# Kernel optimization log

Hardware: AMD Instinct MI355X
Metric: run time of the kernel (lower is better)

The kernel has to match this reference:

```python
import jax, jax.numpy as jnp
import numpy as np

N, NFEAT, NHID, NCLASS, NHEADS = 4096, 512, 64, 40, 8
ALPHA = 0.2
NEG = -9e15


def setup_inputs() -> dict:
    key = jax.random.key(0)
    ks = jax.random.split(key, 6)
    x = jax.random.normal(ks[0], (N, NFEAT), dtype=jnp.float32)
    adj = jax.random.randint(ks[1], (2, N, N), 0, 2, dtype=jnp.int32)
    # Xavier-ish scaled params
    W1 = jax.random.normal(ks[2], (NHEADS, NFEAT, NHID), dtype=jnp.float32) * (1.0 / np.sqrt(NFEAT))
    a1 = jax.random.normal(ks[3], (NHEADS, 2, NHID), dtype=jnp.float32) * (1.0 / np.sqrt(2 * NHID))
    Wo = jax.random.normal(ks[4], (NHEADS * NHID, NCLASS), dtype=jnp.float32) * (1.0 / np.sqrt(NHEADS * NHID))
    ao = jax.random.normal(ks[5], (2, NCLASS), dtype=jnp.float32) * (1.0 / np.sqrt(2 * NCLASS))
    return {"x": x, "adj": adj, "W1": W1, "a1": a1, "Wo": Wo, "ao": ao}


def _gat_layer(h, adj_mask, W, a_src, a_dst, concat):
    # h: [N,F]; W: [...,F,F']; a_src/a_dst: [...,F']
    if W.ndim == 3:  # multi-head: [H,F,F']
        Wh = jnp.einsum('nf,hfd->hnd', h, W)              # [H,N,F']
        f1 = jnp.einsum('hnd,hd->hn', Wh, a_src)           # [H,N]
        f2 = jnp.einsum('hnd,hd->hn', Wh, a_dst)
        e = jax.nn.leaky_relu(f1[:, :, None] + f2[:, None, :], ALPHA)  # [H,N,N]
        e = jnp.where(adj_mask[None], e, NEG)
        att = jax.nn.softmax(e, axis=-1)
        out = jnp.einsum('hnm,hmd->hnd', att, Wh)          # [H,N,F']
    else:
        Wh = h @ W                                         # [N,F']
        f1 = Wh @ a_src
        f2 = Wh @ a_dst
        e = jax.nn.leaky_relu(f1[:, None] + f2[None, :], ALPHA)
        e = jnp.where(adj_mask, e, NEG)
        att = jax.nn.softmax(e, axis=-1)
        out = att @ Wh
    return jax.nn.elu(out) if concat else out


def reference(x, adj, W1, a1, Wo, ao):
    adj1 = adj[1] > 0
    adj0 = adj[0] > 0
    # layer 1: NHEADS heads, concat=True
    h = _gat_layer(x, adj1, W1, a1[:, 0], a1[:, 1], concat=True)   # [H,N,NHID]
    h = jnp.transpose(h, (1, 0, 2)).reshape(x.shape[0], -1)        # [N, H*NHID]
    # output layer: concat=False, then outer ELU + log_softmax
    out = _gat_layer(h, adj0, Wo, ao[0], ao[1], concat=False)      # [N, NCLASS]
    out = jax.nn.elu(out)
    return jax.nn.log_softmax(out, axis=1)
```

## Files before the change

kernel.cpp:

```cpp
#include <hip/hip_runtime.h>
#include <hip/hip_bf16.h>

#define N      4096
#define NFEAT  512
#define NHID   64
#define NHEADS 8
#define NCLASS 40
#define ALPHA  0.2f
#define LOG2E  1.44269504f

typedef unsigned short u16;
typedef unsigned int   u32;
typedef __attribute__((ext_vector_type(8))) short bf16x8;
typedef __attribute__((ext_vector_type(4))) float f32x4;

__device__ __forceinline__ float b2f(u16 u) {
    return __uint_as_float(((u32)u) << 16);
}
__device__ __forceinline__ u32 rnd_hi(float f) {
    u32 u = __float_as_uint(f);
    return u + 0x7FFFu + ((u >> 16) & 1u);
}
__device__ __forceinline__ u32 pk2(float lo, float hi) {
    __hip_bfloat162 h = __float22bfloat162_rn(make_float2(lo, hi));
    return *(u32*)&h;
}
__device__ __forceinline__ u16 f2b(float f) {
    return (u16)(rnd_hi(f) >> 16);
}
__device__ __forceinline__ float mexp(int m, float t) {
    return m ? __builtin_amdgcn_exp2f(fmaxf(t, ALPHA * t)) : 0.f;
}
__device__ __forceinline__ bf16x8 ones_frag() {
    union { u16 u[8]; bf16x8 v; } o;
    #pragma unroll
    for (int j = 0; j < 8; ++j) o.u[j] = 0x3F80;
    return o.v;
}

__global__ __launch_bounds__(256) void kcx(const float* __restrict__ x,
                                           u16* __restrict__ xb) {
    const int g = blockIdx.x * 256 + threadIdx.x;
    const size_t base = (size_t)g * 8;
    float4 v0 = *(const float4*)&x[base];
    float4 v1 = *(const float4*)&x[base + 4];
    uint4 o;
    o.x = pk2(v0.x, v0.y); o.y = pk2(v0.z, v0.w);
    o.z = pk2(v1.x, v1.y); o.w = pk2(v1.z, v1.w);
    *(uint4*)&xb[base] = o;
}

__global__ __launch_bounds__(256) void kcw(const float* __restrict__ W1,
                                           u16* __restrict__ W1b) {
    __shared__ float ts[64 * 68];
    const int t  = threadIdx.x;
    const int f0 = blockIdx.x * 64;
    const int h  = blockIdx.y;
    #pragma unroll
    for (int i = 0; i < 4; ++i) {
        int flat = t + 256 * i;
        int row = flat >> 4;
        int c4  = (flat & 15) * 4;
        *(float4*)&ts[row * 68 + c4] =
            *(const float4*)&W1[((size_t)h * 512 + f0 + row) * 64 + c4];
    }
    __syncthreads();
    const int d  = t >> 2;
    const int fs = (t & 3) * 16;
    u32 p[8];
    #pragma unroll
    for (int j = 0; j < 8; ++j)
        p[j] = pk2(ts[(fs + 2 * j) * 68 + d], ts[(fs + 2 * j + 1) * 68 + d]);
    u32* dst = (u32*)&W1b[((size_t)(h * 64 + d)) * 512 + f0 + fs];
    *(uint4*)dst       = make_uint4(p[0], p[1], p[2], p[3]);
    *(uint4*)(dst + 4) = make_uint4(p[4], p[5], p[6], p[7]);
}

__global__ __launch_bounds__(256, 4) void k1m_gemm1(const u16* __restrict__ xb,
                                                    const u16* __restrict__ W1b,
                                                    const float* __restrict__ a1,
                                                    u16* __restrict__ Wh1T,
                                                    float* __restrict__ F1,
                                                    float* __restrict__ F2) {
    __shared__ u16 xs[64 * 72];
    __shared__ u16 wvs[64 * 72];
    const int t    = threadIdx.x;
    const int n0   = blockIdx.x * 64;
    const int h    = blockIdx.y;
    const int lane = t & 63;
    const int l15  = lane & 15;
    const int q    = lane >> 4;
    const int wrow = (t >> 6) * 16;
    f32x4 acc[4];
    #pragma unroll
    for (int df = 0; df < 4; ++df)
        #pragma unroll
        for (int r = 0; r < 4; ++r) acc[df][r] = 0.f;
    for (int f0 = 0; f0 < 512; f0 += 64) {
        uint4 sx[2], sw[2];
        #pragma unroll
        for (int i = 0; i < 2; ++i) {
            int flat = t + 256 * i;
            int row = flat >> 3;
            int c8  = (flat & 7) * 8;
            sx[i] = *(const uint4*)&xb[(size_t)(n0 + row) * 512 + f0 + c8];
            sw[i] = *(const uint4*)&W1b[((size_t)(h * 64 + row)) * 512 + f0 + c8];
        }
        __syncthreads();
        #pragma unroll
        for (int i = 0; i < 2; ++i) {
            int flat = t + 256 * i;
            int row = flat >> 3;
            int c8  = (flat & 7) * 8;
            *(uint4*)&xs[row * 72 + c8]  = sx[i];
            *(uint4*)&wvs[row * 72 + c8] = sw[i];
        }
        __syncthreads();
        #pragma unroll
        for (int ks = 0; ks < 2; ++ks) {
            int k0 = ks * 32 + q * 8;
            bf16x8 a = *(const bf16x8*)&xs[(wrow + l15) * 72 + k0];
            #pragma unroll
            for (int df = 0; df < 4; ++df) {
                bf16x8 b = *(const bf16x8*)&wvs[(df * 16 + l15) * 72 + k0];
                acc[df] = __builtin_amdgcn_mfma_f32_16x16x32_bf16(a, b, acc[df], 0, 0, 0);
            }
        }
    }
    #pragma unroll
    for (int df = 0; df < 4; ++df) {
        uint2 o;
        o.x = pk2(acc[df][0], acc[df][1]);
        o.y = pk2(acc[df][2], acc[df][3]);
        *(uint2*)&Wh1T[((size_t)(h * 64 + df * 16 + l15)) * 4096 + n0 + wrow + q * 4] = o;
    }
    float a1v[4], a2v[4];
    #pragma unroll
    for (int df = 0; df < 4; ++df) {
        a1v[df] = a1[h * 128 + df * 16 + l15];
        a2v[df] = a1[h * 128 + 64 + df * 16 + l15];
    }
    #pragma unroll
    for (int r = 0; r < 4; ++r) {
        float s1 = 0.f, s2 = 0.f;
        #pragma unroll
        for (int df = 0; df < 4; ++df) {
            s1 += acc[df][r] * a1v[df];
            s2 += acc[df][r] * a2v[df];
        }
        #pragma unroll
        for (int off = 8; off >= 1; off >>= 1) {
            s1 += __shfl_xor(s1, off);
            s2 += __shfl_xor(s2, off);
        }
        if (l15 == 0) {
            int n = n0 + wrow + q * 4 + r;
            F1[h * 4096 + n] = s1 * LOG2E;
            F2[h * 4096 + n] = s2 * LOG2E;
        }
    }
}

__global__ __launch_bounds__(256, 4) void k3_attn1(const int* __restrict__ adj1,
                                                   const u16* __restrict__ Wh1T,
                                                   const float* __restrict__ F1,
                                                   const float* __restrict__ F2,
                                                   float* __restrict__ pacc1,
                                                   float* __restrict__ pz1) {
    __shared__ u16  wbf[64 * 136];
    __shared__ u16  whT[64 * 136];
    __shared__ float f1s[64];
    const int t     = threadIdx.x;
    const int n0    = blockIdx.x * 64;
    const int h     = blockIdx.y;
    const int chunk = blockIdx.z;
    const int lane  = t & 63;
    const int l15   = lane & 15;
    const int q     = lane >> 4;
    const int wrow  = (t >> 6) * 16;
    const int c4    = (t & 31) * 4;
    const int rg    = t >> 5;
    const bf16x8 bones = ones_frag();
    if (t < 64) f1s[t] = F1[h * N + n0 + t];
    f32x4 acc[5];
    #pragma unroll
    for (int df = 0; df < 5; ++df)
        #pragma unroll
        for (int r = 0; r < 4; ++r) acc[df][r] = 0.f;

    const int mbeg = chunk * 2048;
    int4 aprev[8];
    #pragma unroll
    for (int i = 0; i < 8; ++i)
        aprev[i] = *(const int4*)&adj1[(size_t)(n0 + rg + 8 * i) * N + mbeg + c4];
    __syncthreads();

    for (int m0 = mbeg; m0 < mbeg + 2048; m0 += 128) {
        float4 F2v = *(const float4*)&F2[h * N + m0 + c4];
        #pragma unroll
        for (int i = 0; i < 8; ++i) {
            int rr = rg + 8 * i;
            int4 a4 = aprev[i];
            float f1v = f1s[rr];
            float w0 = mexp(a4.x, f1v + F2v.x);
            float w1 = mexp(a4.y, f1v + F2v.y);
            float w2 = mexp(a4.z, f1v + F2v.z);
            float w3 = mexp(a4.w, f1v + F2v.w);
            uint2 pk;
            pk.x = pk2(w0, w1);
            pk.y = pk2(w2, w3);
            *(uint2*)&wbf[rr * 136 + c4] = pk;
        }
        int mn = (m0 + 128 < mbeg + 2048) ? m0 + 128 : mbeg;
        #pragma unroll
        for (int i = 0; i < 8; ++i)
            aprev[i] = *(const int4*)&adj1[(size_t)(n0 + rg + 8 * i) * N + mn + c4];
        #pragma unroll
        for (int i = 0; i < 4; ++i) {
            int flat = t + 256 * i;
            int row = flat >> 4;
            int c8  = (flat & 15) * 8;
            *(uint4*)&whT[row * 136 + c8] =
                *(const uint4*)&Wh1T[((size_t)(h * 64 + row)) * 4096 + m0 + c8];
        }
        __syncthreads();
        #pragma unroll
        for (int ks = 0; ks < 4; ++ks) {
            int k0 = ks * 32 + q * 8;
            bf16x8 a = *(const bf16x8*)&wbf[(wrow + l15) * 136 + k0];
            #pragma unroll
            for (int df = 0; df < 4; ++df) {
                bf16x8 b = *(const bf16x8*)&whT[(df * 16 + l15) * 136 + k0];
                acc[df] = __builtin_amdgcn_mfma_f32_16x16x32_bf16(a, b, acc[df], 0, 0, 0);
            }
            acc[4] = __builtin_amdgcn_mfma_f32_16x16x32_bf16(a, bones, acc[4], 0, 0, 0);
        }
        __syncthreads();
    }
    const size_t rowbase = (size_t)(chunk * 8 + h) * 4096 + n0;
    #pragma unroll
    for (int r = 0; r < 4; ++r) {
        int nl = wrow + q * 4 + r;
        if (l15 == 0) pz1[rowbase + nl] = acc[4][r];
        #pragma unroll
        for (int df = 0; df < 4; ++df)
            pacc1[(rowbase + nl) * 64 + df * 16 + l15] = acc[df][r];
    }
}

__global__ __launch_bounds__(256) void k3b_norm(const float* __restrict__ pacc1,
                                                const float* __restrict__ pz1,
                                                float* __restrict__ h1) {
    const int g = blockIdx.x * 256 + threadIdx.x;
    const int d = g & 63;
    const int h = (g >> 6) & 7;
    const int n = g >> 9;
    const size_t i0 = (size_t)h * 4096 + n;
    float s = pacc1[i0 * 64 + d] + pacc1[(i0 + 8 * 4096) * 64 + d];
    float z = pz1[i0] + pz1[i0 + 8 * 4096];
    float v = s / fmaxf(z, 1e-30f);
    h1[(size_t)n * 512 + h * 64 + d] = v > 0.f ? v : __expf(v) - 1.f;
}

__global__ __launch_bounds__(256) void k4_gemm2(const float* __restrict__ h1,
                                                const float* __restrict__ Wo,
                                                const float* __restrict__ ao,
                                                float* __restrict__ F1o,
                                                float* __restrict__ F2o,
                                                u16* __restrict__ Wh2T) {
    const int t = threadIdx.x;
    const int c = t & 63;
    const int n = blockIdx.x * 4 + (t >> 6);
    float acc = 0.f;
    if (c < NCLASS) {
        const float* hrow = &h1[(size_t)n * 512];
        #pragma unroll 8
        for (int f = 0; f < 512; ++f)
            acc += hrow[f] * Wo[f * NCLASS + c];
        Wh2T[(size_t)c * 4096 + n] = f2b(acc);
    }
    float s1 = (c < NCLASS) ? acc * ao[c] : 0.f;
    float s2 = (c < NCLASS) ? acc * ao[NCLASS + c] : 0.f;
    #pragma unroll
    for (int off = 32; off >= 1; off >>= 1) {
        s1 += __shfl_xor(s1, off);
        s2 += __shfl_xor(s2, off);
    }
    if (c == 0) {
        F1o[n] = s1 * LOG2E;
        F2o[n] = s2 * LOG2E;
    }
}

__global__ __launch_bounds__(256, 5) void k5a_attn2(const int* __restrict__ adj0,
                                                    const u16* __restrict__ Wh2T,
                                                    const float* __restrict__ F1o,
                                                    const float* __restrict__ F2o,
                                                    float* __restrict__ pacc,
                                                    float* __restrict__ pz) {
    __shared__ u16  wbf[64 * 136];
    __shared__ u16  whT[48 * 136];
    __shared__ float f1s[64];
    const int t     = threadIdx.x;
    const int n0    = blockIdx.x * 64;
    const int chunk = blockIdx.y;
    const int mbase = chunk * 256;
    const int lane  = t & 63;
    const int l15   = lane & 15;
    const int q     = lane >> 4;
    const int wrow  = (t >> 6) * 16;
    const int c4    = (t & 31) * 4;
    const int rg    = t >> 5;
    const bf16x8 bones = ones_frag();
    if (t < 64) f1s[t] = F1o[n0 + t];
    #pragma unroll
    for (int i = 0; i < 5; ++i) {
        int idx = t + 256 * i;
        if (idx < 1088) whT[40 * 136 + idx] = 0;
    }
    f32x4 acc[4];
    #pragma unroll
    for (int df = 0; df < 4; ++df)
        #pragma unroll
        for (int r = 0; r < 4; ++r) acc[df][r] = 0.f;
    int4 aprev[8];
    #pragma unroll
    for (int i = 0; i < 8; ++i)
        aprev[i] = *(const int4*)&adj0[(size_t)(n0 + rg + 8 * i) * N + mbase + c4];
    __syncthreads();

    for (int mt = 0; mt < 2; ++mt) {
        int m0 = mbase + mt * 128;
        float4 F2v = *(const float4*)&F2o[m0 + c4];
        #pragma unroll
        for (int i = 0; i < 8; ++i) {
            int rr = rg + 8 * i;
            int4 a4 = aprev[i];
            float f1v = f1s[rr];
            float w0 = mexp(a4.x, f1v + F2v.x);
            float w1 = mexp(a4.y, f1v + F2v.y);
            float w2 = mexp(a4.z, f1v + F2v.z);
            float w3 = mexp(a4.w, f1v + F2v.w);
            uint2 pk;
            pk.x = pk2(w0, w1);
            pk.y = pk2(w2, w3);
            *(uint2*)&wbf[rr * 136 + c4] = pk;
        }
        int mn = mbase + ((mt + 1) & 1) * 128;
        #pragma unroll
        for (int i = 0; i < 8; ++i)
            aprev[i] = *(const int4*)&adj0[(size_t)(n0 + rg + 8 * i) * N + mn + c4];
        #pragma unroll
        for (int i = 0; i < 3; ++i) {
            int flat = t + 256 * i;
            if (flat < 640) {
                int row = flat >> 4;
                int c8  = (flat & 15) * 8;
                *(uint4*)&whT[row * 136 + c8] =
                    *(const uint4*)&Wh2T[(size_t)row * 4096 + m0 + c8];
            }
        }
        __syncthreads();
        #pragma unroll
        for (int ks = 0; ks < 4; ++ks) {
            int k0 = ks * 32 + q * 8;
            bf16x8 a = *(const bf16x8*)&wbf[(wrow + l15) * 136 + k0];
            #pragma unroll
            for (int df = 0; df < 3; ++df) {
                bf16x8 b = *(const bf16x8*)&whT[(df * 16 + l15) * 136 + k0];
                acc[df] = __builtin_amdgcn_mfma_f32_16x16x32_bf16(a, b, acc[df], 0, 0, 0);
            }
            acc[3] = __builtin_amdgcn_mfma_f32_16x16x32_bf16(a, bones, acc[3], 0, 0, 0);
        }
        __syncthreads();
    }
    #pragma unroll
    for (int r = 0; r < 4; ++r) {
        int n = n0 + wrow + q * 4 + r;
        if (l15 == 0) pz[(size_t)chunk * N + n] = acc[3][r];
        #pragma unroll
        for (int df = 0; df < 3; ++df) {
            int c = df * 16 + l15;
            if (c < NCLASS)
                pacc[((size_t)chunk * N + n) * NCLASS + c] = acc[df][r];
        }
    }
}

__global__ __launch_bounds__(256) void k5b_final(const float* __restrict__ pacc,
                                                 const float* __restrict__ pz,
                                                 float* __restrict__ out) {
    const int t = threadIdx.x;
    const int lane = t & 63;
    const int n = blockIdx.x * 4 + (t >> 6);
    float s = 0.f, Z = 0.f;
    #pragma unroll
    for (int ch = 0; ch < 16; ++ch) {
        Z += pz[(size_t)ch * N + n];
        if (lane < NCLASS) s += pacc[(size_t)(ch * N + n) * NCLASS + lane];
    }
    float v;
    if (lane < NCLASS) {
        v = s / fmaxf(Z, 1e-30f);
        v = v > 0.f ? v : __expf(v) - 1.f;
    } else {
        v = -INFINITY;
    }
    float mx = v;
    #pragma unroll
    for (int off = 32; off >= 1; off >>= 1) mx = fmaxf(mx, __shfl_xor(mx, off));
    float ex = (lane < NCLASS) ? __expf(v - mx) : 0.f;
    #pragma unroll
    for (int off = 32; off >= 1; off >>= 1) ex += __shfl_xor(ex, off);
    float lse = mx + __logf(ex);
    if (lane < NCLASS) out[(size_t)n * NCLASS + lane] = v - lse;
}

extern "C" void kernel_launch(void* const* d_in, const int* in_sizes, int n_in,
                              void* d_out, int out_size, void* d_ws, size_t ws_size,
                              hipStream_t stream) {
    const float* x   = (const float*)d_in[0];
    const int*   adj = (const int*)d_in[1];
    const float* W1  = (const float*)d_in[2];
    const float* a1  = (const float*)d_in[3];
    const float* Wo  = (const float*)d_in[4];
    const float* ao  = (const float*)d_in[5];

    float* ws    = (float*)d_ws;
    float* h1    = ws;
    float* F1    = h1 + 2097152;
    float* F2    = F1 + 32768;
    float* F1o   = F2 + 32768;
    float* F2o   = F1o + 4096;
    float* pz    = F2o + 4096;
    float* pz1   = pz + 65536;
    u16*   Wh1T  = (u16*)(pz1 + 65536);
    u16*   Wh2T  = Wh1T + 2097152;
    float* R     = (float*)(Wh2T + 163840);
    u16*   xb    = (u16*)R;
    u16*   W1b   = xb + 2097152;
    float* pacc1 = R;
    float* pacc  = R;

    const int* adj0 = adj;
    const int* adj1 = adj + (size_t)N * N;

    hipLaunchKernelGGL(kcx,       dim3(1024),     dim3(256), 0, stream, x, xb);
    hipLaunchKernelGGL(kcw,       dim3(8, 8),     dim3(256), 0, stream, W1, W1b);
    hipLaunchKernelGGL(k1m_gemm1, dim3(64, 8),    dim3(256), 0, stream, xb, W1b, a1, Wh1T, F1, F2);
    hipLaunchKernelGGL(k3_attn1,  dim3(64, 8, 2), dim3(256), 0, stream, adj1, Wh1T, F1, F2, pacc1, pz1);
    hipLaunchKernelGGL(k3b_norm,  dim3(8192),     dim3(256), 0, stream, pacc1, pz1, h1);
    hipLaunchKernelGGL(k4_gemm2,  dim3(1024),     dim3(256), 0, stream, h1, Wo, ao, F1o, F2o, Wh2T);
    hipLaunchKernelGGL(k5a_attn2, dim3(64, 16),   dim3(256), 0, stream, adj0, Wh2T, F1o, F2o, pacc, pz);
    hipLaunchKernelGGL(k5b_final, dim3(1024),     dim3(256), 0, stream, pacc, pz, (float*)d_out);
}
```

Baseline: 333.5 us.

## Compute attention weights directly in MFMA A-fragment registers, skipping LDS staging

In both attention kernels each lane now loads the adjacency entries matching its own MFMA A-operand slot, computes the exponentiated weights in registers and packs them straight into bf16x8 fragments. This removes the shared-memory round trip for the weight tile. The Wh tile is prefetched into registers one step ahead, and F2 is cached in LDS for the whole chunk. Adjacency reads per lane become 32-byte row segments rather than coalesced 128-column strips, which may cost memory efficiency. The attn2 launch bound drops to 4 blocks per SM.

```diff
diff --git a/kernel.cpp b/kernel.cpp
--- a/kernel.cpp
+++ b/kernel.cpp
@@ -167,9 +167,8 @@
                                                    const float* __restrict__ F2,
                                                    float* __restrict__ pacc1,
                                                    float* __restrict__ pz1) {
-    __shared__ u16  wbf[64 * 136];
-    __shared__ u16  whT[64 * 136];
-    __shared__ float f1s[64];
+    __shared__ u16   whT[64 * 136];
+    __shared__ float f2s[2048];
     const int t     = threadIdx.x;
     const int n0    = blockIdx.x * 64;
     const int h     = blockIdx.y;
@@ -178,62 +177,78 @@
     const int l15   = lane & 15;
     const int q     = lane >> 4;
     const int wrow  = (t >> 6) * 16;
-    const int c4    = (t & 31) * 4;
-    const int rg    = t >> 5;
+    const int row   = wrow + l15;
     const bf16x8 bones = ones_frag();
-    if (t < 64) f1s[t] = F1[h * N + n0 + t];
+    const int mbeg  = chunk * 2048;
+    const float f1v = F1[h * N + n0 + row];
+
+    {
+        float4 fa = *(const float4*)&F2[h * N + mbeg + t * 8];
+        float4 fb = *(const float4*)&F2[h * N + mbeg + t * 8 + 4];
+        *(float4*)&f2s[t * 8]     = fa;
+        *(float4*)&f2s[t * 8 + 4] = fb;
+    }
+
+    const int srow = t >> 4;
+    const int sc8  = (t & 15) * 8;
+    const u16* wbase = Wh1T + ((size_t)(h * 64 + srow)) * 4096 + sc8;
+    const int* adjq  = adj1 + (size_t)(n0 + row) * N + q * 8;
+
+    uint4 bw[4];
+    int4  aj[4][2];
+    auto pref_bw = [&](int m0) {
+        #pragma unroll
+        for (int i = 0; i < 4; ++i)
+            bw[i] = *(const uint4*)(wbase + (size_t)(16 * i) * 4096 + m0);
+    };
+    auto pref_adj = [&](int m0) {
+        #pragma unroll
+        for (int ks = 0; ks < 4; ++ks) {
+            aj[ks][0] = *(const int4*)(adjq + m0 + ks * 32);
+            aj[ks][1] = *(const int4*)(adjq + m0 + ks * 32 + 4);
+        }
+    };
+
     f32x4 acc[5];
     #pragma unroll
     for (int df = 0; df < 5; ++df)
         #pragma unroll
         for (int r = 0; r < 4; ++r) acc[df][r] = 0.f;
 
-    const int mbeg = chunk * 2048;
-    int4 aprev[8];
-    #pragma unroll
-    for (int i = 0; i < 8; ++i)
-        aprev[i] = *(const int4*)&adj1[(size_t)(n0 + rg + 8 * i) * N + mbeg + c4];
-    __syncthreads();
-
-    for (int m0 = mbeg; m0 < mbeg + 2048; m0 += 128) {
-        float4 F2v = *(const float4*)&F2[h * N + m0 + c4];
-        #pragma unroll
-        for (int i = 0; i < 8; ++i) {
-            int rr = rg + 8 * i;
-            int4 a4 = aprev[i];
-            float f1v = f1s[rr];
-            float w0 = mexp(a4.x, f1v + F2v.x);
-            float w1 = mexp(a4.y, f1v + F2v.y);
-            float w2 = mexp(a4.z, f1v + F2v.z);
-            float w3 = mexp(a4.w, f1v + F2v.w);
-            uint2 pk;
-            pk.x = pk2(w0, w1);
-            pk.y = pk2(w2, w3);
-            *(uint2*)&wbf[rr * 136 + c4] = pk;
-        }
-        int mn = (m0 + 128 < mbeg + 2048) ? m0 + 128 : mbeg;
-        #pragma unroll
-        for (int i = 0; i < 8; ++i)
-            aprev[i] = *(const int4*)&adj1[(size_t)(n0 + rg + 8 * i) * N + mn + c4];
-        #pragma unroll
-        for (int i = 0; i < 4; ++i) {
-            int flat = t + 256 * i;
-            int row = flat >> 4;
-            int c8  = (flat & 15) * 8;
-            *(uint4*)&whT[row * 136 + c8] =
-                *(const uint4*)&Wh1T[((size_t)(h * 64 + row)) * 4096 + m0 + c8];
-        }
-        __syncthreads();
-        #pragma unroll
-        for (int ks = 0; ks < 4; ++ks) {
-            int k0 = ks * 32 + q * 8;
-            bf16x8 a = *(const bf16x8*)&wbf[(wrow + l15) * 136 + k0];
+    pref_bw(mbeg);
+    pref_adj(mbeg);
+
+    for (int it = 0; it < 16; ++it) {
+        const int mrel  = it * 128;
+        const int mnext = mbeg + ((it < 15) ? mrel + 128 : 0);
+        #pragma unroll
+        for (int i = 0; i < 4; ++i)
+            *(uint4*)&whT[(srow + 16 * i) * 136 + sc8] = bw[i];
+        __syncthreads();
+        pref_bw(mnext);
+        bf16x8 af[4];
+        #pragma unroll
+        for (int ks = 0; ks < 4; ++ks) {
+            const float* f2p = &f2s[mrel + ks * 32 + q * 8];
+            float4 fa = *(const float4*)f2p;
+            float4 fb = *(const float4*)(f2p + 4);
+            int4 a0 = aj[ks][0], a1 = aj[ks][1];
+            union { u32 u[4]; bf16x8 v; } fr;
+            fr.u[0] = pk2(mexp(a0.x, f1v + fa.x), mexp(a0.y, f1v + fa.y));
+            fr.u[1] = pk2(mexp(a0.z, f1v + fa.z), mexp(a0.w, f1v + fa.w));
+            fr.u[2] = pk2(mexp(a1.x, f1v + fb.x), mexp(a1.y, f1v + fb.y));
+            fr.u[3] = pk2(mexp(a1.z, f1v + fb.z), mexp(a1.w, f1v + fb.w));
+            af[ks] = fr.v;
+        }
+        pref_adj(mnext);
+        #pragma unroll
+        for (int ks = 0; ks < 4; ++ks) {
             #pragma unroll
             for (int df = 0; df < 4; ++df) {
-                bf16x8 b = *(const bf16x8*)&whT[(df * 16 + l15) * 136 + k0];
-                acc[df] = __builtin_amdgcn_mfma_f32_16x16x32_bf16(a, b, acc[df], 0, 0, 0);
+                bf16x8 b = *(const bf16x8*)&whT[(df * 16 + l15) * 136 + ks * 32 + q * 8];
+                acc[df] = __builtin_amdgcn_mfma_f32_16x16x32_bf16(af[ks], b, acc[df], 0, 0, 0);
             }
-            acc[4] = __builtin_amdgcn_mfma_f32_16x16x32_bf16(a, bones, acc[4], 0, 0, 0);
+            acc[4] = __builtin_amdgcn_mfma_f32_16x16x32_bf16(af[ks], bones, acc[4], 0, 0, 0);
         }
         __syncthreads();
     }
@@ -292,15 +307,14 @@
     }
 }
 
-__global__ __launch_bounds__(256, 5) void k5a_attn2(const int* __restrict__ adj0,
+__global__ __launch_bounds__(256, 4) void k5a_attn2(const int* __restrict__ adj0,
                                                     const u16* __restrict__ Wh2T,
                                                     const float* __restrict__ F1o,
                                                     const float* __restrict__ F2o,
                                                     float* __restrict__ pacc,
                                                     float* __restrict__ pz) {
-    __shared__ u16  wbf[64 * 136];
-    __shared__ u16  whT[48 * 136];
-    __shared__ float f1s[64];
+    __shared__ u16   whT[48 * 136];
+    __shared__ float f2s[256];
     const int t     = threadIdx.x;
     const int n0    = blockIdx.x * 64;
     const int chunk = blockIdx.y;
@@ -309,68 +323,80 @@
     const int l15   = lane & 15;
     const int q     = lane >> 4;
     const int wrow  = (t >> 6) * 16;
-    const int c4    = (t & 31) * 4;
-    const int rg    = t >> 5;
+    const int row   = wrow + l15;
     const bf16x8 bones = ones_frag();
-    if (t < 64) f1s[t] = F1o[n0 + t];
+    const float f1v = F1o[n0 + row];
+
+    if (t < 64) *(float4*)&f2s[t * 4] = *(const float4*)&F2o[mbase + t * 4];
     #pragma unroll
     for (int i = 0; i < 5; ++i) {
         int idx = t + 256 * i;
         if (idx < 1088) whT[40 * 136 + idx] = 0;
     }
+
+    const int srow = t >> 4;
+    const int sc8  = (t & 15) * 8;
+    const u16* wbase = Wh2T + (size_t)srow * 4096 + sc8;
+    const int* adjq  = adj0 + (size_t)(n0 + row) * N + q * 8;
+
+    uint4 bw[3];
+    int4  aj[4][2];
+    auto pref_bw = [&](int m0) {
+        #pragma unroll
+        for (int i = 0; i < 3; ++i)
+            if (srow + 16 * i < 40)
+                bw[i] = *(const uint4*)(wbase + (size_t)(16 * i) * 4096 + m0);
+    };
+    auto pref_adj = [&](int m0) {
+        #pragma unroll
+        for (int ks = 0; ks < 4; ++ks) {
+            aj[ks][0] = *(const int4*)(adjq + m0 + ks * 32);
+            aj[ks][1] = *(const int4*)(adjq + m0 + ks * 32 + 4);
+        }
+    };
+
     f32x4 acc[4];
     #pragma unroll
     for (int df = 0; df < 4; ++df)
         #pragma unroll
         for (int r = 0; r < 4; ++r) acc[df][r] = 0.f;
-    int4 aprev[8];
-    #pragma unroll
-    for (int i = 0; i < 8; ++i)
-        aprev[i] = *(const int4*)&adj0[(size_t)(n0 + rg + 8 * i) * N + mbase + c4];
-    __syncthreads();
-
+
+    pref_bw(mbase);
+    pref_adj(mbase);
+
+    #pragma unroll
     for (int mt = 0; mt < 2; ++mt) {
-        int m0 = mbase + mt * 128;
-        float4 F2v = *(const float4*)&F2o[m0 + c4];
-        #pragma unroll
-        for (int i = 0; i < 8; ++i) {
-            int rr = rg + 8 * i;
-            int4 a4 = aprev[i];
-            float f1v = f1s[rr];
-            float w0 = mexp(a4.x, f1v + F2v.x);
-            float w1 = mexp(a4.y, f1v + F2v.y);
-            float w2 = mexp(a4.z, f1v + F2v.z);
-            float w3 = mexp(a4.w, f1v + F2v.w);
-            uint2 pk;
-            pk.x = pk2(w0, w1);
-            pk.y = pk2(w2, w3);
-            *(uint2*)&wbf[rr * 136 + c4] = pk;
-        }
-        int mn = mbase + ((mt + 1) & 1) * 128;
-        #pragma unroll
-        for (int i = 0; i < 8; ++i)
-            aprev[i] = *(const int4*)&adj0[(size_t)(n0 + rg + 8 * i) * N + mn + c4];
-        #pragma unroll
-        for (int i = 0; i < 3; ++i) {
-            int flat = t + 256 * i;
-            if (flat < 640) {
-                int row = flat >> 4;
-                int c8  = (flat & 15) * 8;
-                *(uint4*)&whT[row * 136 + c8] =
-                    *(const uint4*)&Wh2T[(size_t)row * 4096 + m0 + c8];
-            }
-        }
-        __syncthreads();
-        #pragma unroll
-        for (int ks = 0; ks < 4; ++ks) {
-            int k0 = ks * 32 + q * 8;
-            bf16x8 a = *(const bf16x8*)&wbf[(wrow + l15) * 136 + k0];
+        const int mrel  = mt * 128;
+        const int mnext = mbase + ((mt + 1) & 1) * 128;
+        #pragma unroll
+        for (int i = 0; i < 3; ++i)
+            if (srow + 16 * i < 40)
+                *(uint4*)&whT[(srow + 16 * i) * 136 + sc8] = bw[i];
+        __syncthreads();
+        pref_bw(mnext);
+        bf16x8 af[4];
+        #pragma unroll
+        for (int ks = 0; ks < 4; ++ks) {
+            const float* f2p = &f2s[mrel + ks * 32 + q * 8];
+            float4 fa = *(const float4*)f2p;
+            float4 fb = *(const float4*)(f2p + 4);
+            int4 a0 = aj[ks][0], a1 = aj[ks][1];
+            union { u32 u[4]; bf16x8 v; } fr;
+            fr.u[0] = pk2(mexp(a0.x, f1v + fa.x), mexp(a0.y, f1v + fa.y));
+            fr.u[1] = pk2(mexp(a0.z, f1v + fa.z), mexp(a0.w, f1v + fa.w));
+            fr.u[2] = pk2(mexp(a1.x, f1v + fb.x), mexp(a1.y, f1v + fb.y));
+            fr.u[3] = pk2(mexp(a1.z, f1v + fb.z), mexp(a1.w, f1v + fb.w));
+            af[ks] = fr.v;
+        }
+        pref_adj(mnext);
+        #pragma unroll
+        for (int ks = 0; ks < 4; ++ks) {
             #pragma unroll
             for (int df = 0; df < 3; ++df) {
-                bf16x8 b = *(const bf16x8*)&whT[(df * 16 + l15) * 136 + k0];
-                acc[df] = __builtin_amdgcn_mfma_f32_16x16x32_bf16(a, b, acc[df], 0, 0, 0);
+                bf16x8 b = *(const bf16x8*)&whT[(df * 16 + l15) * 136 + ks * 32 + q * 8];
+                acc[df] = __builtin_amdgcn_mfma_f32_16x16x32_bf16(af[ks], b, acc[df], 0, 0, 0);
             }
-            acc[3] = __builtin_amdgcn_mfma_f32_16x16x32_bf16(a, bones, acc[3], 0, 0, 0);
+            acc[3] = __builtin_amdgcn_mfma_f32_16x16x32_bf16(af[ks], bones, acc[3], 0, 0, 0);
         }
         __syncthreads();
     }
```

After: 402.8 us. +20.8%, slower.

## Register-prefetch next tile and use raw barriers without vmcnt drain

Applied to the files above, without the earlier changes.

In the projection kernel and both attention kernels, the next iteration's global loads (x/W tiles, Wh tiles, adjacency, F2) are now issued into registers before the current tile's MFMA work. __syncthreads is replaced by an lgkmcnt wait plus s_barrier fenced with sched_barrier, so the barrier no longer waits for outstanding global loads and those loads can overlap compute. This adds register pressure, and k5a_attn2's launch bounds occupancy hint drops from 5 to 4 to make room.

```diff
diff --git a/kernel.cpp b/kernel.cpp
--- a/kernel.cpp
+++ b/kernel.cpp
@@ -96,26 +96,33 @@
     for (int df = 0; df < 4; ++df)
         #pragma unroll
         for (int r = 0; r < 4; ++r) acc[df][r] = 0.f;
+
+    uint4 sx[2], sw[2];
+    const int srow = t >> 3;
+    const int sc8  = (t & 7) * 8;
+    const u16* xb0 = xb + (size_t)(n0 + srow) * 512 + sc8;
+    const u16* wb0 = W1b + ((size_t)(h * 64 + srow)) * 512 + sc8;
+    #pragma unroll
+    for (int i = 0; i < 2; ++i) {
+        sx[i] = *(const uint4*)(xb0 + (size_t)(32 * i) * 512);
+        sw[i] = *(const uint4*)(wb0 + (size_t)(32 * i) * 512);
+    }
     for (int f0 = 0; f0 < 512; f0 += 64) {
-        uint4 sx[2], sw[2];
         #pragma unroll
         for (int i = 0; i < 2; ++i) {
-            int flat = t + 256 * i;
-            int row = flat >> 3;
-            int c8  = (flat & 7) * 8;
-            sx[i] = *(const uint4*)&xb[(size_t)(n0 + row) * 512 + f0 + c8];
-            sw[i] = *(const uint4*)&W1b[((size_t)(h * 64 + row)) * 512 + f0 + c8];
-        }
-        __syncthreads();
+            *(uint4*)&xs[(srow + 32 * i) * 72 + sc8]  = sx[i];
+            *(uint4*)&wvs[(srow + 32 * i) * 72 + sc8] = sw[i];
+        }
+        const int fn = (f0 + 64 < 512) ? f0 + 64 : 0;
         #pragma unroll
         for (int i = 0; i < 2; ++i) {
-            int flat = t + 256 * i;
-            int row = flat >> 3;
-            int c8  = (flat & 7) * 8;
-            *(uint4*)&xs[row * 72 + c8]  = sx[i];
-            *(uint4*)&wvs[row * 72 + c8] = sw[i];
-        }
-        __syncthreads();
+            sx[i] = *(const uint4*)(xb0 + (size_t)(32 * i) * 512 + fn);
+            sw[i] = *(const uint4*)(wb0 + (size_t)(32 * i) * 512 + fn);
+        }
+        asm volatile("s_waitcnt lgkmcnt(0)" ::: "memory");
+        __builtin_amdgcn_sched_barrier(0);
+        __builtin_amdgcn_s_barrier();
+        __builtin_amdgcn_sched_barrier(0);
         #pragma unroll
         for (int ks = 0; ks < 2; ++ks) {
             int k0 = ks * 32 + q * 8;
@@ -126,6 +133,9 @@
                 acc[df] = __builtin_amdgcn_mfma_f32_16x16x32_bf16(a, b, acc[df], 0, 0, 0);
             }
         }
+        __builtin_amdgcn_sched_barrier(0);
+        __builtin_amdgcn_s_barrier();
+        __builtin_amdgcn_sched_barrier(0);
     }
     #pragma unroll
     for (int df = 0; df < 4; ++df) {
@@ -180,27 +190,41 @@
     const int wrow  = (t >> 6) * 16;
     const int c4    = (t & 31) * 4;
     const int rg    = t >> 5;
+    const int srow  = t >> 4;
+    const int sc8   = (t & 15) * 8;
     const bf16x8 bones = ones_frag();
+    const int mbeg  = chunk * 2048;
     if (t < 64) f1s[t] = F1[h * N + n0 + t];
-    f32x4 acc[5];
+
+    const u16*   wb0  = Wh1T + ((size_t)(h * 64 + srow)) * 4096 + sc8;
+    const int*   adjp = adj1 + (size_t)(n0 + rg) * N + c4;
+    const float* f2p  = F2 + (size_t)h * N + c4;
+
+    uint4  bw[4];
+    int4   aj[8];
+    float4 f2n;
+    f32x4  acc[5];
     #pragma unroll
     for (int df = 0; df < 5; ++df)
         #pragma unroll
         for (int r = 0; r < 4; ++r) acc[df][r] = 0.f;
 
-    const int mbeg = chunk * 2048;
-    int4 aprev[8];
+    #pragma unroll
+    for (int i = 0; i < 4; ++i)
+        bw[i] = *(const uint4*)(wb0 + (size_t)(16 * i) * 4096 + mbeg);
     #pragma unroll
     for (int i = 0; i < 8; ++i)
-        aprev[i] = *(const int4*)&adj1[(size_t)(n0 + rg + 8 * i) * N + mbeg + c4];
+        aj[i] = *(const int4*)(adjp + (size_t)(8 * i) * N + mbeg);
+    f2n = *(const float4*)(f2p + mbeg);
     __syncthreads();
 
-    for (int m0 = mbeg; m0 < mbeg + 2048; m0 += 128) {
-        float4 F2v = *(const float4*)&F2[h * N + m0 + c4];
+    for (int it = 0; it < 16; ++it) {
+        const int m0 = mbeg + it * 128;
+        const float4 F2v = f2n;
         #pragma unroll
         for (int i = 0; i < 8; ++i) {
             int rr = rg + 8 * i;
-            int4 a4 = aprev[i];
+            int4 a4 = aj[i];
             float f1v = f1s[rr];
             float w0 = mexp(a4.x, f1v + F2v.x);
             float w1 = mexp(a4.y, f1v + F2v.y);
@@ -211,19 +235,21 @@
             pk.y = pk2(w2, w3);
             *(uint2*)&wbf[rr * 136 + c4] = pk;
         }
-        int mn = (m0 + 128 < mbeg + 2048) ? m0 + 128 : mbeg;
+        #pragma unroll
+        for (int i = 0; i < 4; ++i)
+            *(uint4*)&whT[(srow + 16 * i) * 136 + sc8] = bw[i];
+        const int mn = (it < 15) ? m0 + 128 : mbeg;
+        #pragma unroll
+        for (int i = 0; i < 4; ++i)
+            bw[i] = *(const uint4*)(wb0 + (size_t)(16 * i) * 4096 + mn);
         #pragma unroll
         for (int i = 0; i < 8; ++i)
-            aprev[i] = *(const int4*)&adj1[(size_t)(n0 + rg + 8 * i) * N + mn + c4];
-        #pragma unroll
-        for (int i = 0; i < 4; ++i) {
-            int flat = t + 256 * i;
-            int row = flat >> 4;
-            int c8  = (flat & 15) * 8;
-            *(uint4*)&whT[row * 136 + c8] =
-                *(const uint4*)&Wh1T[((size_t)(h * 64 + row)) * 4096 + m0 + c8];
-        }
-        __syncthreads();
+            aj[i] = *(const int4*)(adjp + (size_t)(8 * i) * N + mn);
+        f2n = *(const float4*)(f2p + mn);
+        asm volatile("s_waitcnt lgkmcnt(0)" ::: "memory");
+        __builtin_amdgcn_sched_barrier(0);
+        __builtin_amdgcn_s_barrier();
+        __builtin_amdgcn_sched_barrier(0);
         #pragma unroll
         for (int ks = 0; ks < 4; ++ks) {
             int k0 = ks * 32 + q * 8;
@@ -235,7 +261,9 @@
             }
             acc[4] = __builtin_amdgcn_mfma_f32_16x16x32_bf16(a, bones, acc[4], 0, 0, 0);
         }
-        __syncthreads();
+        __builtin_amdgcn_sched_barrier(0);
+        __builtin_amdgcn_s_barrier();
+        __builtin_amdgcn_sched_barrier(0);
     }
     const size_t rowbase = (size_t)(chunk * 8 + h) * 4096 + n0;
     #pragma unroll
@@ -292,7 +320,7 @@
     }
 }
 
-__global__ __launch_bounds__(256, 5) void k5a_attn2(const int* __restrict__ adj0,
+__global__ __launch_bounds__(256, 4) void k5a_attn2(const int* __restrict__ adj0,
                                                     const u16* __restrict__ Wh2T,
                                                     const float* __restrict__ F1o,
                                                     const float* __restrict__ F2o,
@@ -311,6 +339,8 @@
     const int wrow  = (t >> 6) * 16;
     const int c4    = (t & 31) * 4;
     const int rg    = t >> 5;
+    const int srow  = t >> 4;
+    const int sc8   = (t & 15) * 8;
     const bf16x8 bones = ones_frag();
     if (t < 64) f1s[t] = F1o[n0 + t];
     #pragma unroll
@@ -318,24 +348,37 @@
         int idx = t + 256 * i;
         if (idx < 1088) whT[40 * 136 + idx] = 0;
     }
-    f32x4 acc[4];
+
+    const u16*   wb0  = Wh2T + (size_t)srow * 4096 + sc8;
+    const int*   adjp = adj0 + (size_t)(n0 + rg) * N + c4;
+    const float* f2p  = F2o + c4;
+
+    uint4  bw[3];
+    int4   aj[8];
+    float4 f2n;
+    f32x4  acc[4];
     #pragma unroll
     for (int df = 0; df < 4; ++df)
         #pragma unroll
         for (int r = 0; r < 4; ++r) acc[df][r] = 0.f;
-    int4 aprev[8];
+
+    #pragma unroll
+    for (int i = 0; i < 3; ++i)
+        if (srow + 16 * i < 40)
+            bw[i] = *(const uint4*)(wb0 + (size_t)(16 * i) * 4096 + mbase);
     #pragma unroll
     for (int i = 0; i < 8; ++i)
-        aprev[i] = *(const int4*)&adj0[(size_t)(n0 + rg + 8 * i) * N + mbase + c4];
+        aj[i] = *(const int4*)(adjp + (size_t)(8 * i) * N + mbase);
+    f2n = *(const float4*)(f2p + mbase);
     __syncthreads();
 
+    #pragma unroll
     for (int mt = 0; mt < 2; ++mt) {
-        int m0 = mbase + mt * 128;
-        float4 F2v = *(const float4*)&F2o[m0 + c4];
+        const float4 F2v = f2n;
         #pragma unroll
         for (int i = 0; i < 8; ++i) {
             int rr = rg + 8 * i;
-            int4 a4 = aprev[i];
+            int4 a4 = aj[i];
             float f1v = f1s[rr];
             float w0 = mexp(a4.x, f1v + F2v.x);
             float w1 = mexp(a4.y, f1v + F2v.y);
@@ -346,21 +389,23 @@
             pk.y = pk2(w2, w3);
             *(uint2*)&wbf[rr * 136 + c4] = pk;
         }
-        int mn = mbase + ((mt + 1) & 1) * 128;
+        #pragma unroll
+        for (int i = 0; i < 3; ++i)
+            if (srow + 16 * i < 40)
+                *(uint4*)&whT[(srow + 16 * i) * 136 + sc8] = bw[i];
+        const int mn = mbase + ((mt + 1) & 1) * 128;
+        #pragma unroll
+        for (int i = 0; i < 3; ++i)
+            if (srow + 16 * i < 40)
+                bw[i] = *(const uint4*)(wb0 + (size_t)(16 * i) * 4096 + mn);
         #pragma unroll
         for (int i = 0; i < 8; ++i)
-            aprev[i] = *(const int4*)&adj0[(size_t)(n0 + rg + 8 * i) * N + mn + c4];
-        #pragma unroll
-        for (int i = 0; i < 3; ++i) {
-            int flat = t + 256 * i;
-            if (flat < 640) {
-                int row = flat >> 4;
-                int c8  = (flat & 15) * 8;
-                *(uint4*)&whT[row * 136 + c8] =
-                    *(const uint4*)&Wh2T[(size_t)row * 4096 + m0 + c8];
-            }
-        }
-        __syncthreads();
+            aj[i] = *(const int4*)(adjp + (size_t)(8 * i) * N + mn);
+        f2n = *(const float4*)(f2p + mn);
+        asm volatile("s_waitcnt lgkmcnt(0)" ::: "memory");
+        __builtin_amdgcn_sched_barrier(0);
+        __builtin_amdgcn_s_barrier();
+        __builtin_amdgcn_sched_barrier(0);
         #pragma unroll
         for (int ks = 0; ks < 4; ++ks) {
             int k0 = ks * 32 + q * 8;
@@ -372,7 +417,9 @@
             }
             acc[3] = __builtin_amdgcn_mfma_f32_16x16x32_bf16(a, bones, acc[3], 0, 0, 0);
         }
-        __syncthreads();
+        __builtin_amdgcn_sched_barrier(0);
+        __builtin_amdgcn_s_barrier();
+        __builtin_amdgcn_sched_barrier(0);
     }
     #pragma unroll
     for (int r = 0; r < 4; ++r) {
```

Result: slower. 374.7 us (+12.3%).
